# Optimization experiments

Measured on AMD Instinct MI355X. Metric: run time of the kernel, lower is better.

Reference implementation:

```python
import jax, jax.numpy as jnp
import numpy as np
from jax import lax

B, C, H, W = 4, 64, 64, 64
CH = C // 2  # edge_detect hidden channels
BN_EPS = 1e-5


def conv1x1(x, w, b):
    # x: (B,C,H,W), w: (O,C), b: (O,)
    return jnp.einsum('bchw,oc->bohw', x, w) + b[None, :, None, None]


def setup_inputs() -> dict:
    key = jax.random.key(0)
    ks = jax.random.split(key, 12)
    s = 1.0 / np.sqrt(C)
    inp = {
        'x': jax.random.normal(ks[0], (B, C, H, W), jnp.float32),
        'Wq': jax.random.normal(ks[1], (C, C), jnp.float32) * s,
        'bq': jnp.zeros((C,), jnp.float32),
        'Wk': jax.random.normal(ks[2], (C, C), jnp.float32) * s,
        'bk': jnp.zeros((C,), jnp.float32),
        'Wv': jax.random.normal(ks[3], (C, C), jnp.float32) * s,
        'bv': jnp.zeros((C,), jnp.float32),
        'We1': jax.random.normal(ks[4], (CH, C, 3, 3), jnp.float32) * (1.0 / np.sqrt(C * 9)),
        'be1': jnp.zeros((CH,), jnp.float32),
        'bn_w': jnp.ones((CH,), jnp.float32),
        'bn_b': jnp.zeros((CH,), jnp.float32),
        'bn_mean': jnp.zeros((CH,), jnp.float32),
        'bn_var': jnp.ones((CH,), jnp.float32),
        'We2': jax.random.normal(ks[5], (1, CH), jnp.float32) * (1.0 / np.sqrt(CH)),
        'be2': jnp.zeros((1,), jnp.float32),
        'gamma': jax.random.normal(ks[6], (1,), jnp.float32) * 0.1,
        'beta': jax.random.normal(ks[7], (1,), jnp.float32) * 0.1,
    }
    return inp


def reference(x, Wq, bq, Wk, bk, Wv, bv, We1, be1, bn_w, bn_b, bn_mean, bn_var, We2, be2, gamma, beta):
    b, c, h, w = x.shape
    hw = h * w
    q = conv1x1(x, Wq, bq).reshape(b, c, hw).transpose(0, 2, 1)  # (B,HW,C)
    k = conv1x1(x, Wk, bk).reshape(b, c, hw)                      # (B,C,HW)
    v = conv1x1(x, Wv, bv).reshape(b, c, hw)                      # (B,C,HW)

    energy = jnp.einsum('bnc,bcm->bnm', q, k)                      # (B,HW,HW)
    attention = jax.nn.softmax(energy, axis=-1)

    # edge_detect: 3x3 conv -> BN (eval stats) -> ReLU -> 1x1 conv -> sigmoid
    e = lax.conv_general_dilated(x, We1, (1, 1), 'SAME',
                                 dimension_numbers=('NCHW', 'OIHW', 'NCHW'))
    e = e + be1[None, :, None, None]
    e = (e - bn_mean[None, :, None, None]) * jax.lax.rsqrt(bn_var + BN_EPS)[None, :, None, None]
    e = e * bn_w[None, :, None, None] + bn_b[None, :, None, None]
    e = jax.nn.relu(e)
    e = conv1x1(e, We2, be2)                                       # (B,1,H,W)
    edge = jax.nn.sigmoid(e).reshape(b, 1, hw)                     # (B,1,HW)

    fa = attention * (1.0 + beta[0] * edge)                        # broadcast over query dim
    denom = jnp.maximum(jnp.sum(jnp.abs(fa), axis=2, keepdims=True), 1e-12)
    fa = fa / denom                                                # L1 renorm along keys

    out = jnp.einsum('bcm,bnm->bcn', v, fa).reshape(b, c, h, w)
    return gamma[0] * out + x
```

## Files before the change

### kernel.cpp

```cpp
#include <hip/hip_runtime.h>
#include <hip/hip_bf16.h>

typedef unsigned short u16;
typedef __attribute__((ext_vector_type(8))) __bf16 bf16x8;
typedef __attribute__((ext_vector_type(4))) float f32x4;
typedef __attribute__((ext_vector_type(16))) float f32x16;


#define NSPLIT 8

__device__ __forceinline__ u16 f2bf(float f) {
    unsigned u = __builtin_bit_cast(unsigned, f);
    u += 0x7FFFu + ((u >> 16) & 1u);
    return (u16)(u >> 16);
}
__device__ __forceinline__ float bf2f(u16 v) {
    unsigned u = ((unsigned)v) << 16;
    return __builtin_bit_cast(float, u);
}

__global__ __launch_bounds__(256) void qkv_edge_kernel(
    const float* __restrict__ x,
    const float* __restrict__ Wq, const float* __restrict__ bq,
    const float* __restrict__ Wk, const float* __restrict__ bk,
    const float* __restrict__ Wv, const float* __restrict__ bv,
    const float* __restrict__ We1, const float* __restrict__ be1,
    const float* __restrict__ bn_w, const float* __restrict__ bn_b,
    const float* __restrict__ bn_mean, const float* __restrict__ bn_var,
    const float* __restrict__ We2, const float* __restrict__ be2,
    const float* __restrict__ beta,
    u16* __restrict__ Qt, u16* __restrict__ Kt, u16* __restrict__ Vm,
    float* __restrict__ wkey)
{
    __shared__ __align__(16) u16 sm[33280];
    const int t = threadIdx.x;
    const int wv = t >> 6, lane = t & 63;
    const int quad = lane >> 4, l15 = lane & 15;

    if (blockIdx.x < 256) {
        u16* Wl   = sm;
        u16* xt_s = sm + 13824;
        u16* vt   = sm + 13824 + 4224;
        const int b = blockIdx.x >> 6;
        const int n0 = (blockIdx.x & 63) << 6;

        const float* Wmat[3] = {Wq, Wk, Wv};
#pragma unroll
        for (int m = 0; m < 3; ++m)
#pragma unroll
            for (int i = 0; i < 4; ++i) {
                int u = t + i * 256;
                float4 w4 = *reinterpret_cast<const float4*>(Wmat[m] + u * 4);
                int row = u >> 4, col = (u & 15) * 4;
                uint2 pk;
                pk.x = (unsigned)f2bf(w4.x) | ((unsigned)f2bf(w4.y) << 16);
                pk.y = (unsigned)f2bf(w4.z) | ((unsigned)f2bf(w4.w) << 16);
                *reinterpret_cast<uint2*>(&Wl[(m * 64 + row) * 72 + col]) = pk;
            }
        for (int i = 0; i < 16; ++i) {
            int lin = t + i * 256;
            int c = lin >> 6, nn = lin & 63;
            xt_s[nn * 66 + c] = f2bf(x[(size_t)(b * 64 + c) * 4096 + n0 + nn]);
        }
        __syncthreads();

        bf16x8 bx[2];
#pragma unroll
        for (int h = 0; h < 2; ++h)
            bx[h] = *reinterpret_cast<const bf16x8*>(
                &xt_s[(wv * 16 + l15) * 66 + h * 32 + quad * 8]);

        f32x4 d[3][4];
#pragma unroll
        for (int m = 0; m < 3; ++m)
#pragma unroll
            for (int mt = 0; mt < 4; ++mt) d[m][mt] = (f32x4){0.f, 0.f, 0.f, 0.f};

#pragma unroll
        for (int h = 0; h < 2; ++h)
#pragma unroll
            for (int m = 0; m < 3; ++m)
#pragma unroll
                for (int mt = 0; mt < 4; ++mt) {
                    bf16x8 af = *reinterpret_cast<const bf16x8*>(
                        &Wl[(m * 64 + mt * 16 + l15) * 72 + h * 32 + quad * 8]);
                    d[m][mt] = __builtin_amdgcn_mfma_f32_16x16x32_bf16(af, bx[h], d[m][mt], 0, 0, 0);
                }

        const float* bias[3] = {bq, bk, bv};
        const float L2E = 1.44269504f;
#pragma unroll
        for (int m = 0; m < 3; ++m)
#pragma unroll
            for (int mt = 0; mt < 4; ++mt) {
                float4 bi = *reinterpret_cast<const float4*>(bias[m] + mt * 16 + quad * 4);
                d[m][mt][0] += bi.x; d[m][mt][1] += bi.y; d[m][mt][2] += bi.z; d[m][mt][3] += bi.w;
                if (m == 0) {
                    d[m][mt][0] *= L2E; d[m][mt][1] *= L2E;
                    d[m][mt][2] *= L2E; d[m][mt][3] *= L2E;
                }
            }

        const int rowchunk = (n0 >> 4) + wv;
#pragma unroll
        for (int m = 0; m < 2; ++m) {
            u16* base = (m == 0 ? Qt : Kt) + (size_t)b * 262144;
#pragma unroll
            for (int mt = 0; mt < 4; ++mt) {
                uint2 pk;
                pk.x = (unsigned)f2bf(d[m][mt][0]) | ((unsigned)f2bf(d[m][mt][1]) << 16);
                pk.y = (unsigned)f2bf(d[m][mt][2]) | ((unsigned)f2bf(d[m][mt][3]) << 16);
                *reinterpret_cast<uint2*>(
                    base + ((size_t)(rowchunk * 8 + mt * 2 + (quad >> 1))) * 128 +
                    l15 * 8 + (quad & 1) * 4) = pk;
            }
        }
#pragma unroll
        for (int mt = 0; mt < 4; ++mt)
#pragma unroll
            for (int r = 0; r < 4; ++r)
                vt[(mt * 16 + quad * 4 + r) * 72 + wv * 16 + l15] = f2bf(d[2][mt][r]);
        __syncthreads();
        {
            u16* Vb_st = Vm + (size_t)b * 262144;
            const int kt = n0 >> 6;
#pragma unroll
            for (int i = 0; i < 2; ++i) {
                int unit = t + i * 256;
                int f = unit >> 7, hq = (unit >> 4) & 7, cl = unit & 15;
                const u16* src = &vt[(f * 16 + cl) * 72 + hq * 8];
                uint4 v4 = *reinterpret_cast<const uint4*>(src);
                *reinterpret_cast<uint4*>(
                    Vb_st + ((size_t)((kt * 4 + f) * 8 + hq)) * 128 + cl * 8) = v4;
            }
        }
    } else {
        u16* Ae_s = sm;
        u16* xr_s = sm + 18688;
        const int eb = blockIdx.x - 256;
        const int b = eb >> 6, h = eb & 63;

        if (t < 192) {
            int kh = t / 64, rem = t & 63;
            int col = (rem >> 5) * 65, ci2 = (rem & 31) * 2;
            *reinterpret_cast<unsigned*>(&xr_s[(kh * 66 + col) * 72 + ci2]) = 0u;
        }
#pragma unroll
        for (int i = 0; i < 18; ++i) {
            int u = t + i * 256;
            int ch = u / 144;
            int rem = u - ch * 144;
            int p = rem >> 4, cig = (rem & 15) * 4;
            const float* src = We1 + ch * 576 + cig * 9 + p;
            float a = src[0], b2 = src[9], c2 = src[18], d2 = src[27];
            uint2 pk;
            pk.x = (unsigned)f2bf(a) | ((unsigned)f2bf(b2) << 16);
            pk.y = (unsigned)f2bf(c2) | ((unsigned)f2bf(d2) << 16);
            *reinterpret_cast<uint2*>(&Ae_s[ch * 584 + p * 64 + cig]) = pk;
        }
#pragma unroll
        for (int i = 0; i < 12; ++i) {
            int u = t + i * 256;
            int w = u & 63, cig = (u >> 6) & 15, kh = u >> 10;
            int hs = h + kh - 1;
            float v0 = 0.f, v1 = 0.f, v2 = 0.f, v3 = 0.f;
            if ((unsigned)hs < 64u) {
                const float* src = x + ((size_t)(b * 64 + cig * 4) * 64 + hs) * 64 + w;
                v0 = src[0]; v1 = src[4096]; v2 = src[8192]; v3 = src[12288];
            }
            uint2 pk;
            pk.x = (unsigned)f2bf(v0) | ((unsigned)f2bf(v1) << 16);
            pk.y = (unsigned)f2bf(v2) | ((unsigned)f2bf(v3) << 16);
            *reinterpret_cast<uint2*>(&xr_s[(kh * 66 + w + 1) * 72 + cig * 4]) = pk;
        }
        __syncthreads();

        f32x4 e[2];
        e[0] = (f32x4){0.f, 0.f, 0.f, 0.f};
        e[1] = (f32x4){0.f, 0.f, 0.f, 0.f};
#pragma unroll
        for (int p = 0; p < 9; ++p) {
            const int kh = p / 3, kw = p - kh * 3;
#pragma unroll
            for (int half = 0; half < 2; ++half) {
                bf16x8 bfr = *reinterpret_cast<const bf16x8*>(
                    &xr_s[(kh * 66 + wv * 16 + l15 + kw) * 72 + half * 32 + quad * 8]);
#pragma unroll
                for (int mt = 0; mt < 2; ++mt) {
                    bf16x8 af = *reinterpret_cast<const bf16x8*>(
                        &Ae_s[(mt * 16 + l15) * 584 + p * 64 + half * 32 + quad * 8]);
                    e[mt] = __builtin_amdgcn_mfma_f32_16x16x32_bf16(af, bfr, e[mt], 0, 0, 0);
                }
            }
        }
        float partial = 0.f;
#pragma unroll
        for (int mt = 0; mt < 2; ++mt) {
            float4 bw = *reinterpret_cast<const float4*>(bn_w    + mt * 16 + quad * 4);
            float4 bb = *reinterpret_cast<const float4*>(bn_b    + mt * 16 + quad * 4);
            float4 bm = *reinterpret_cast<const float4*>(bn_mean + mt * 16 + quad * 4);
            float4 bv2 = *reinterpret_cast<const float4*>(bn_var + mt * 16 + quad * 4);
            float4 b1 = *reinterpret_cast<const float4*>(be1     + mt * 16 + quad * 4);
            float4 w2 = *reinterpret_cast<const float4*>(We2     + mt * 16 + quad * 4);
            float sc, sh;
            sc = bw.x * rsqrtf(bv2.x + 1e-5f); sh = (b1.x - bm.x) * sc + bb.x;
            partial += fmaxf(e[mt][0] * sc + sh, 0.f) * w2.x;
            sc = bw.y * rsqrtf(bv2.y + 1e-5f); sh = (b1.y - bm.y) * sc + bb.y;
            partial += fmaxf(e[mt][1] * sc + sh, 0.f) * w2.y;
            sc = bw.z * rsqrtf(bv2.z + 1e-5f); sh = (b1.z - bm.z) * sc + bb.z;
            partial += fmaxf(e[mt][2] * sc + sh, 0.f) * w2.z;
            sc = bw.w * rsqrtf(bv2.w + 1e-5f); sh = (b1.w - bm.w) * sc + bb.w;
            partial += fmaxf(e[mt][3] * sc + sh, 0.f) * w2.w;
        }
        partial += __shfl_xor(partial, 16);
        partial += __shfl_xor(partial, 32);
        if (lane < 16) {
            float s = partial + be2[0];
            float sg = 1.f / (1.f + __expf(-s));
            wkey[(size_t)b * 4096 + h * 64 + wv * 16 + lane] =
                __log2f(fmaxf(1.f + beta[0] * sg, 1e-20f)) - 17.3123405f;
        }
    }
}

__global__ __launch_bounds__(256, 2) void attn_kernel(
    const u16* __restrict__ Qt, const u16* __restrict__ Kt,
    const u16* __restrict__ Vm, const float* __restrict__ lwkey,
    u16* __restrict__ O_part, float* __restrict__ l_part)
{
    constexpr int KT_ITERS = 64 / NSPLIT;
    const int bid = ((blockIdx.x & 7) << 7) + (blockIdx.x >> 3);
    const int t = threadIdx.x;
    const int qi = bid / NSPLIT;
    const int split = bid % NSPLIT;
    const int b = qi >> 5;
    const int n0 = (qi & 31) << 7;
    const int wv = t >> 6, lane = t & 63;
    const int l31 = lane & 31, hi = lane >> 5;
    const int i4 = (lane >> 4) & 1, l15 = lane & 15;

    const int kvoff = i4 * 1024 + hi * 128 + l15 * 8;
    const u16* Qb = Qt + (size_t)b * 262144;
    const u16* Kp = Kt + (size_t)b * 262144 + (size_t)(split * KT_ITERS) * 4096 + kvoff;
    const u16* Vp = Vm + (size_t)b * 262144 + (size_t)(split * KT_ITERS) * 4096 + kvoff;
    const float* lwp = lwkey + (size_t)b * 4096 + (split * KT_ITERS) * 64 + hi * 4;

    bf16x8 qf[4];
#pragma unroll
    for (int kc = 0; kc < 4; ++kc)
        qf[kc] = __builtin_bit_cast(bf16x8, *reinterpret_cast<const uint4*>(
            Qb + (size_t)(((n0 >> 4) + wv * 2) * 1024) + kvoff + kc * 256));

    f32x16 o[2];
#pragma unroll
    for (int ct = 0; ct < 2; ++ct)
#pragma unroll
        for (int i = 0; i < 16; ++i) o[ct][i] = 0.f;
    float lacc = 0.f;

    for (int kt = 0; kt < KT_ITERS; ++kt) {
        uint4 pbu[2][2];
#pragma unroll
        for (int tl = 0; tl < 2; ++tl) {
            uint4 k0 = *reinterpret_cast<const uint4*>(Kp + tl * 2048);
            uint4 k1 = *reinterpret_cast<const uint4*>(Kp + tl * 2048 + 256);
            uint4 k2 = *reinterpret_cast<const uint4*>(Kp + tl * 2048 + 512);
            uint4 k3 = *reinterpret_cast<const uint4*>(Kp + tl * 2048 + 768);
            float4 lw0 = *reinterpret_cast<const float4*>(lwp + tl * 32);
            float4 lw1 = *reinterpret_cast<const float4*>(lwp + tl * 32 + 8);
            float4 lw2 = *reinterpret_cast<const float4*>(lwp + tl * 32 + 16);
            float4 lw3 = *reinterpret_cast<const float4*>(lwp + tl * 32 + 24);

            f32x16 s;
#pragma unroll
            for (int i = 0; i < 16; ++i) s[i] = 0.f;
            __builtin_amdgcn_s_setprio(1);
            s = __builtin_amdgcn_mfma_f32_32x32x16_bf16(__builtin_bit_cast(bf16x8, k0), qf[0], s, 0, 0, 0);
            s = __builtin_amdgcn_mfma_f32_32x32x16_bf16(__builtin_bit_cast(bf16x8, k1), qf[1], s, 0, 0, 0);
            s = __builtin_amdgcn_mfma_f32_32x32x16_bf16(__builtin_bit_cast(bf16x8, k2), qf[2], s, 0, 0, 0);
            s = __builtin_amdgcn_mfma_f32_32x32x16_bf16(__builtin_bit_cast(bf16x8, k3), qf[3], s, 0, 0, 0);
            __builtin_amdgcn_s_setprio(0);

            float p[16];
            p[0]  = exp2f(s[0]  + lw0.x); p[1]  = exp2f(s[1]  + lw0.y);
            p[2]  = exp2f(s[2]  + lw0.z); p[3]  = exp2f(s[3]  + lw0.w);
            p[4]  = exp2f(s[4]  + lw1.x); p[5]  = exp2f(s[5]  + lw1.y);
            p[6]  = exp2f(s[6]  + lw1.z); p[7]  = exp2f(s[7]  + lw1.w);
            p[8]  = exp2f(s[8]  + lw2.x); p[9]  = exp2f(s[9]  + lw2.y);
            p[10] = exp2f(s[10] + lw2.z); p[11] = exp2f(s[11] + lw2.w);
            p[12] = exp2f(s[12] + lw3.x); p[13] = exp2f(s[13] + lw3.y);
            p[14] = exp2f(s[14] + lw3.z); p[15] = exp2f(s[15] + lw3.w);
            float t0 = (p[0] + p[1]) + (p[2] + p[3]);
            float t1 = (p[4] + p[5]) + (p[6] + p[7]);
            float t2 = (p[8] + p[9]) + (p[10] + p[11]);
            float t3 = (p[12] + p[13]) + (p[14] + p[15]);
            lacc += (t0 + t1) + (t2 + t3);

#pragma unroll
            for (int kc2 = 0; kc2 < 2; ++kc2) {
                int a0, a1, b0, b1;
                asm("v_cvt_pk_bf16_f32 %0, %1, %2" : "=v"(a0) : "v"(p[kc2 * 8 + 0]), "v"(p[kc2 * 8 + 1]));
                asm("v_cvt_pk_bf16_f32 %0, %1, %2" : "=v"(a1) : "v"(p[kc2 * 8 + 2]), "v"(p[kc2 * 8 + 3]));
                asm("v_cvt_pk_bf16_f32 %0, %1, %2" : "=v"(b0) : "v"(p[kc2 * 8 + 4]), "v"(p[kc2 * 8 + 5]));
                asm("v_cvt_pk_bf16_f32 %0, %1, %2" : "=v"(b1) : "v"(p[kc2 * 8 + 6]), "v"(p[kc2 * 8 + 7]));
                auto swA = __builtin_amdgcn_permlane32_swap(a0, b0, false, false);
                auto swB = __builtin_amdgcn_permlane32_swap(a1, b1, false, false);
                uint4 fr;
                fr.x = (unsigned)swA[0];
                fr.y = (unsigned)swB[0];
                fr.z = (unsigned)swA[1];
                fr.w = (unsigned)swB[1];
                pbu[tl][kc2] = fr;
            }
        }

#pragma unroll
        for (int ct = 0; ct < 2; ++ct) {
            uint4 v0 = *reinterpret_cast<const uint4*>(Vp + ct * 2048);
            uint4 v1 = *reinterpret_cast<const uint4*>(Vp + ct * 2048 + 256);
            uint4 v2 = *reinterpret_cast<const uint4*>(Vp + ct * 2048 + 512);
            uint4 v3 = *reinterpret_cast<const uint4*>(Vp + ct * 2048 + 768);
            __builtin_amdgcn_s_setprio(1);
            o[ct] = __builtin_amdgcn_mfma_f32_32x32x16_bf16(__builtin_bit_cast(bf16x8, v0),
                        __builtin_bit_cast(bf16x8, pbu[0][0]), o[ct], 0, 0, 0);
            o[ct] = __builtin_amdgcn_mfma_f32_32x32x16_bf16(__builtin_bit_cast(bf16x8, v1),
                        __builtin_bit_cast(bf16x8, pbu[0][1]), o[ct], 0, 0, 0);
            o[ct] = __builtin_amdgcn_mfma_f32_32x32x16_bf16(__builtin_bit_cast(bf16x8, v2),
                        __builtin_bit_cast(bf16x8, pbu[1][0]), o[ct], 0, 0, 0);
            o[ct] = __builtin_amdgcn_mfma_f32_32x32x16_bf16(__builtin_bit_cast(bf16x8, v3),
                        __builtin_bit_cast(bf16x8, pbu[1][1]), o[ct], 0, 0, 0);
            __builtin_amdgcn_s_setprio(0);
        }
        Kp += 4096; Vp += 4096; lwp += 64;
    }

    float ltot = lacc + __shfl_xor(lacc, 32);
    if (lane < 32)
        l_part[(size_t)bid * 128 + wv * 32 + lane] = ltot;

    const size_t pbase = (size_t)bid * 8192;
    const int q = wv * 32 + l31;
#pragma unroll
    for (int ct = 0; ct < 2; ++ct)
#pragma unroll
        for (int g = 0; g < 4; ++g) {
            int w0, w1;
            asm("v_cvt_pk_bf16_f32 %0, %1, %2" : "=v"(w0) : "v"(o[ct][4 * g + 0]), "v"(o[ct][4 * g + 1]));
            asm("v_cvt_pk_bf16_f32 %0, %1, %2" : "=v"(w1) : "v"(o[ct][4 * g + 2]), "v"(o[ct][4 * g + 3]));
            uint2 pk2;
            pk2.x = (unsigned)w0;
            pk2.y = (unsigned)w1;
            *reinterpret_cast<uint2*>(
                &O_part[pbase + (size_t)(ct * 8 + g * 2 + hi) * 512 + q * 4]) = pk2;
        }
}

__global__ __launch_bounds__(256) void combine_kernel(
    const u16* __restrict__ O_part, const float* __restrict__ l_part,
    const float* __restrict__ x, const float* __restrict__ g_gamma,
    float* __restrict__ out)
{
    __shared__ float ot[32 * 65];
    __shared__ float ls[32];
    const int t = threadIdx.x;
    const int ab = blockIdx.x >> 2;
    const int sub = blockIdx.x & 3;
    const int b = ab >> 5;
    const int n0 = (ab & 31) << 7;
    const float gamma = g_gamma[0];

#pragma unroll
    for (int i = 0; i < 2; ++i) {
        int idx = t + i * 256;
        int c4 = idx >> 5, ql = idx & 31;
        float a0 = 0.f, a1 = 0.f, a2 = 0.f, a3 = 0.f;
#pragma unroll
        for (int s4 = 0; s4 < NSPLIT; ++s4) {
            uint2 u = *reinterpret_cast<const uint2*>(
                O_part + ((size_t)(ab * NSPLIT + s4)) * 8192 +
                (size_t)c4 * 512 + (sub * 32 + ql) * 4);
            a0 += bf2f((u16)(u.x & 0xFFFF));
            a1 += bf2f((u16)(u.x >> 16));
            a2 += bf2f((u16)(u.y & 0xFFFF));
            a3 += bf2f((u16)(u.y >> 16));
        }
        ot[ql * 65 + c4 * 4 + 0] = a0;
        ot[ql * 65 + c4 * 4 + 1] = a1;
        ot[ql * 65 + c4 * 4 + 2] = a2;
        ot[ql * 65 + c4 * 4 + 3] = a3;
    }
    if (t < 32) {
        float lsum = 0.f;
#pragma unroll
        for (int s4 = 0; s4 < NSPLIT; ++s4)
            lsum += l_part[((size_t)(ab * NSPLIT + s4)) * 128 + sub * 32 + t];
        ls[t] = gamma / fmaxf(lsum, 1e-30f);
    }
    __syncthreads();
    {
        const int c = t >> 2, seg = t & 3;
        const size_t gbase = ((size_t)(b * 64 + c)) * 4096 + n0 + sub * 32 + seg * 8;
#pragma unroll
        for (int j = 0; j < 2; ++j) {
            float4 xv = *reinterpret_cast<const float4*>(&x[gbase + j * 4]);
            float4 rv;
            int nl = seg * 8 + j * 4;
            rv.x = ot[(nl + 0) * 65 + c] * ls[nl + 0] + xv.x;
            rv.y = ot[(nl + 1) * 65 + c] * ls[nl + 1] + xv.y;
            rv.z = ot[(nl + 2) * 65 + c] * ls[nl + 2] + xv.z;
            rv.w = ot[(nl + 3) * 65 + c] * ls[nl + 3] + xv.w;
            *reinterpret_cast<float4*>(&out[gbase + j * 4]) = rv;
        }
    }
}

extern "C" void kernel_launch(void* const* d_in, const int* in_sizes, int n_in,
                              void* d_out, int out_size, void* d_ws, size_t ws_size,
                              hipStream_t stream) {
    const float* x      = (const float*)d_in[0];
    const float* Wq     = (const float*)d_in[1];
    const float* bq     = (const float*)d_in[2];
    const float* Wk     = (const float*)d_in[3];
    const float* bk     = (const float*)d_in[4];
    const float* Wv     = (const float*)d_in[5];
    const float* bv     = (const float*)d_in[6];
    const float* We1    = (const float*)d_in[7];
    const float* be1    = (const float*)d_in[8];
    const float* bn_w   = (const float*)d_in[9];
    const float* bn_b   = (const float*)d_in[10];
    const float* bn_mean= (const float*)d_in[11];
    const float* bn_var = (const float*)d_in[12];
    const float* We2    = (const float*)d_in[13];
    const float* be2    = (const float*)d_in[14];
    const float* gamma  = (const float*)d_in[15];
    const float* beta   = (const float*)d_in[16];

    char* ws = (char*)d_ws;
    const size_t KB = 1024, MB = 1024 * 1024;
    u16*   Qt     = (u16*)ws;
    u16*   Kt     = (u16*)(ws + 2 * MB);
    u16*   Vm     = (u16*)(ws + 4 * MB);
    float* lw     = (float*)(ws + 6 * MB);
    float* l_part = (float*)(ws + 6 * MB + 64 * KB);
    u16*   O_part = (u16*)(ws + 6 * MB + 576 * KB);

    float* out = (float*)d_out;

    qkv_edge_kernel<<<dim3(512), dim3(256), 0, stream>>>(
        x, Wq, bq, Wk, bk, Wv, bv, We1, be1, bn_w, bn_b, bn_mean, bn_var,
        We2, be2, beta, Qt, Kt, Vm, lw);
    attn_kernel<<<dim3(128 * NSPLIT), dim3(256), 0, stream>>>(
        Qt, Kt, Vm, lw, O_part, l_part);
    combine_kernel<<<dim3(512), dim3(256), 0, stream>>>(
        O_part, l_part, x, gamma, out);
}
```

Baseline: 136.9 us.

## Fold key log-weight into QK MFMA and prefetch K/V registers

The per-key log edge weight and the constant offset are now stored as an extra bf16 column block appended to K (5120-element tiles). A constant Q fragment multiplies it inside one additional MFMA, which removes the separate float loads and adds in the softmax loop. K and V fragments are also double-buffered in registers: the next tile's loads are issued right after the current MFMAs. The costs are one extra MFMA per tile, more registers, bf16 rounding of the log weight, and a redundant wraparound prefetch on the last iteration.

```diff
diff --git a/kernel.cpp b/kernel.cpp
--- a/kernel.cpp
+++ b/kernel.cpp
@@ -29,8 +29,7 @@
     const float* __restrict__ bn_mean, const float* __restrict__ bn_var,
     const float* __restrict__ We2, const float* __restrict__ be2,
     const float* __restrict__ beta,
-    u16* __restrict__ Qt, u16* __restrict__ Kt, u16* __restrict__ Vm,
-    float* __restrict__ wkey)
+    u16* __restrict__ Qt, u16* __restrict__ Kt, u16* __restrict__ Vm)
 {
     __shared__ __align__(16) u16 sm[33280];
     const int t = threadIdx.x;
@@ -102,16 +101,27 @@
             }
 
         const int rowchunk = (n0 >> 4) + wv;
-#pragma unroll
-        for (int m = 0; m < 2; ++m) {
-            u16* base = (m == 0 ? Qt : Kt) + (size_t)b * 262144;
+        {
+            u16* baseQ = Qt + (size_t)b * 262144;
 #pragma unroll
             for (int mt = 0; mt < 4; ++mt) {
                 uint2 pk;
-                pk.x = (unsigned)f2bf(d[m][mt][0]) | ((unsigned)f2bf(d[m][mt][1]) << 16);
-                pk.y = (unsigned)f2bf(d[m][mt][2]) | ((unsigned)f2bf(d[m][mt][3]) << 16);
+                pk.x = (unsigned)f2bf(d[0][mt][0]) | ((unsigned)f2bf(d[0][mt][1]) << 16);
+                pk.y = (unsigned)f2bf(d[0][mt][2]) | ((unsigned)f2bf(d[0][mt][3]) << 16);
                 *reinterpret_cast<uint2*>(
-                    base + ((size_t)(rowchunk * 8 + mt * 2 + (quad >> 1))) * 128 +
+                    baseQ + ((size_t)(rowchunk * 8 + mt * 2 + (quad >> 1))) * 128 +
+                    l15 * 8 + (quad & 1) * 4) = pk;
+            }
+        }
+        {
+            u16* baseK = Kt + (size_t)b * 327680 + (size_t)(n0 >> 6) * 5120;
+#pragma unroll
+            for (int mt = 0; mt < 4; ++mt) {
+                uint2 pk;
+                pk.x = (unsigned)f2bf(d[1][mt][0]) | ((unsigned)f2bf(d[1][mt][1]) << 16);
+                pk.y = (unsigned)f2bf(d[1][mt][2]) | ((unsigned)f2bf(d[1][mt][3]) << 16);
+                *reinterpret_cast<uint2*>(
+                    baseK + (size_t)(wv * 8 + mt * 2 + (quad >> 1)) * 128 +
                     l15 * 8 + (quad & 1) * 4) = pk;
             }
         }
@@ -217,15 +227,22 @@
         if (lane < 16) {
             float s = partial + be2[0];
             float sg = 1.f / (1.f + __expf(-s));
-            wkey[(size_t)b * 4096 + h * 64 + wv * 16 + lane] =
-                __log2f(fmaxf(1.f + beta[0] * sg, 1e-20f)) - 17.3123405f;
+            float lwp = __log2f(fmaxf(1.f + beta[0] * sg, 1e-20f));
+            u16* k5 = Kt + (size_t)b * 327680 + (size_t)h * 5120 + 4096 +
+                      (wv >> 1) * 512 + (wv & 1) * 256 + lane * 8;
+            uint4 st0;
+            st0.x = (unsigned)f2bf(lwp) | 0x3F800000u;
+            st0.y = 0u; st0.z = 0u; st0.w = 0u;
+            *reinterpret_cast<uint4*>(k5) = st0;
+            uint4 z; z.x = 0u; z.y = 0u; z.z = 0u; z.w = 0u;
+            *reinterpret_cast<uint4*>(k5 + 128) = z;
         }
     }
 }
 
 __global__ __launch_bounds__(256, 2) void attn_kernel(
     const u16* __restrict__ Qt, const u16* __restrict__ Kt,
-    const u16* __restrict__ Vm, const float* __restrict__ lwkey,
+    const u16* __restrict__ Vm,
     u16* __restrict__ O_part, float* __restrict__ l_part)
 {
     constexpr int KT_ITERS = 64 / NSPLIT;
@@ -240,16 +257,35 @@
     const int i4 = (lane >> 4) & 1, l15 = lane & 15;
 
     const int kvoff = i4 * 1024 + hi * 128 + l15 * 8;
-    const u16* Qb = Qt + (size_t)b * 262144;
-    const u16* Kp = Kt + (size_t)b * 262144 + (size_t)(split * KT_ITERS) * 4096 + kvoff;
-    const u16* Vp = Vm + (size_t)b * 262144 + (size_t)(split * KT_ITERS) * 4096 + kvoff;
-    const float* lwp = lwkey + (size_t)b * 4096 + (split * KT_ITERS) * 64 + hi * 4;
+    const int k5off = i4 * 256 + hi * 128 + l15 * 8;
+    const u16* Qb  = Qt + (size_t)b * 262144;
+    const u16* Ksp = Kt + (size_t)b * 327680 + (size_t)(split * KT_ITERS) * 5120;
+    const u16* Vsp = Vm + (size_t)b * 262144 + (size_t)(split * KT_ITERS) * 4096;
 
     bf16x8 qf[4];
 #pragma unroll
     for (int kc = 0; kc < 4; ++kc)
         qf[kc] = __builtin_bit_cast(bf16x8, *reinterpret_cast<const uint4*>(
             Qb + (size_t)(((n0 >> 4) + wv * 2) * 1024) + kvoff + kc * 256));
+    uint4 qc5u;
+    qc5u.x = hi ? 0u : 0xC18A3F80u;
+    qc5u.y = 0u; qc5u.z = 0u; qc5u.w = 0u;
+    const bf16x8 qc5 = __builtin_bit_cast(bf16x8, qc5u);
+
+    uint4 kf[2][5];
+    uint4 vf[2][4];
+#pragma unroll
+    for (int tl = 0; tl < 2; ++tl) {
+#pragma unroll
+        for (int kc = 0; kc < 4; ++kc)
+            kf[tl][kc] = *reinterpret_cast<const uint4*>(Ksp + tl * 2048 + kc * 256 + kvoff);
+        kf[tl][4] = *reinterpret_cast<const uint4*>(Ksp + 4096 + tl * 512 + k5off);
+    }
+#pragma unroll
+    for (int ct = 0; ct < 2; ++ct)
+#pragma unroll
+        for (int kc = 0; kc < 4; ++kc)
+            vf[ct][kc] = *reinterpret_cast<const uint4*>(Vsp + ct * 2048 + kc * 256 + kvoff);
 
     f32x16 o[2];
 #pragma unroll
@@ -259,43 +295,46 @@
     float lacc = 0.f;
 
     for (int kt = 0; kt < KT_ITERS; ++kt) {
+        f32x16 s0, s1;
+#pragma unroll
+        for (int i = 0; i < 16; ++i) { s0[i] = 0.f; s1[i] = 0.f; }
+        __builtin_amdgcn_s_setprio(1);
+        s0 = __builtin_amdgcn_mfma_f32_32x32x16_bf16(__builtin_bit_cast(bf16x8, kf[0][4]), qc5,   s0, 0, 0, 0);
+        s0 = __builtin_amdgcn_mfma_f32_32x32x16_bf16(__builtin_bit_cast(bf16x8, kf[0][0]), qf[0], s0, 0, 0, 0);
+        s0 = __builtin_amdgcn_mfma_f32_32x32x16_bf16(__builtin_bit_cast(bf16x8, kf[0][1]), qf[1], s0, 0, 0, 0);
+        s0 = __builtin_amdgcn_mfma_f32_32x32x16_bf16(__builtin_bit_cast(bf16x8, kf[0][2]), qf[2], s0, 0, 0, 0);
+        s0 = __builtin_amdgcn_mfma_f32_32x32x16_bf16(__builtin_bit_cast(bf16x8, kf[0][3]), qf[3], s0, 0, 0, 0);
+        s1 = __builtin_amdgcn_mfma_f32_32x32x16_bf16(__builtin_bit_cast(bf16x8, kf[1][4]), qc5,   s1, 0, 0, 0);
+        s1 = __builtin_amdgcn_mfma_f32_32x32x16_bf16(__builtin_bit_cast(bf16x8, kf[1][0]), qf[0], s1, 0, 0, 0);
+        s1 = __builtin_amdgcn_mfma_f32_32x32x16_bf16(__builtin_bit_cast(bf16x8, kf[1][1]), qf[1], s1, 0, 0, 0);
+        s1 = __builtin_amdgcn_mfma_f32_32x32x16_bf16(__builtin_bit_cast(bf16x8, kf[1][2]), qf[2], s1, 0, 0, 0);
+        s1 = __builtin_amdgcn_mfma_f32_32x32x16_bf16(__builtin_bit_cast(bf16x8, kf[1][3]), qf[3], s1, 0, 0, 0);
+        __builtin_amdgcn_s_setprio(0);
+
+        const int ktn = (kt + 1) & (KT_ITERS - 1);
+        {
+            const u16* Kn = Ksp + (size_t)ktn * 5120;
+#pragma unroll
+            for (int tl = 0; tl < 2; ++tl) {
+#pragma unroll
+                for (int kc = 0; kc < 4; ++kc)
+                    kf[tl][kc] = *reinterpret_cast<const uint4*>(Kn + tl * 2048 + kc * 256 + kvoff);
+                kf[tl][4] = *reinterpret_cast<const uint4*>(Kn + 4096 + tl * 512 + k5off);
+            }
+        }
+
         uint4 pbu[2][2];
 #pragma unroll
         for (int tl = 0; tl < 2; ++tl) {
-            uint4 k0 = *reinterpret_cast<const uint4*>(Kp + tl * 2048);
-            uint4 k1 = *reinterpret_cast<const uint4*>(Kp + tl * 2048 + 256);
-            uint4 k2 = *reinterpret_cast<const uint4*>(Kp + tl * 2048 + 512);
-            uint4 k3 = *reinterpret_cast<const uint4*>(Kp + tl * 2048 + 768);
-            float4 lw0 = *reinterpret_cast<const float4*>(lwp + tl * 32);
-            float4 lw1 = *reinterpret_cast<const float4*>(lwp + tl * 32 + 8);
-            float4 lw2 = *reinterpret_cast<const float4*>(lwp + tl * 32 + 16);
-            float4 lw3 = *reinterpret_cast<const float4*>(lwp + tl * 32 + 24);
-
-            f32x16 s;
-#pragma unroll
-            for (int i = 0; i < 16; ++i) s[i] = 0.f;
-            __builtin_amdgcn_s_setprio(1);
-            s = __builtin_amdgcn_mfma_f32_32x32x16_bf16(__builtin_bit_cast(bf16x8, k0), qf[0], s, 0, 0, 0);
-            s = __builtin_amdgcn_mfma_f32_32x32x16_bf16(__builtin_bit_cast(bf16x8, k1), qf[1], s, 0, 0, 0);
-            s = __builtin_amdgcn_mfma_f32_32x32x16_bf16(__builtin_bit_cast(bf16x8, k2), qf[2], s, 0, 0, 0);
-            s = __builtin_amdgcn_mfma_f32_32x32x16_bf16(__builtin_bit_cast(bf16x8, k3), qf[3], s, 0, 0, 0);
-            __builtin_amdgcn_s_setprio(0);
-
+            const f32x16& sv = tl ? s1 : s0;
             float p[16];
-            p[0]  = exp2f(s[0]  + lw0.x); p[1]  = exp2f(s[1]  + lw0.y);
-            p[2]  = exp2f(s[2]  + lw0.z); p[3]  = exp2f(s[3]  + lw0.w);
-            p[4]  = exp2f(s[4]  + lw1.x); p[5]  = exp2f(s[5]  + lw1.y);
-            p[6]  = exp2f(s[6]  + lw1.z); p[7]  = exp2f(s[7]  + lw1.w);
-            p[8]  = exp2f(s[8]  + lw2.x); p[9]  = exp2f(s[9]  + lw2.y);
-            p[10] = exp2f(s[10] + lw2.z); p[11] = exp2f(s[11] + lw2.w);
-            p[12] = exp2f(s[12] + lw3.x); p[13] = exp2f(s[13] + lw3.y);
-            p[14] = exp2f(s[14] + lw3.z); p[15] = exp2f(s[15] + lw3.w);
+#pragma unroll
+            for (int i = 0; i < 16; ++i) p[i] = exp2f(sv[i]);
             float t0 = (p[0] + p[1]) + (p[2] + p[3]);
             float t1 = (p[4] + p[5]) + (p[6] + p[7]);
             float t2 = (p[8] + p[9]) + (p[10] + p[11]);
             float t3 = (p[12] + p[13]) + (p[14] + p[15]);
             lacc += (t0 + t1) + (t2 + t3);
-
 #pragma unroll
             for (int kc2 = 0; kc2 < 2; ++kc2) {
                 int a0, a1, b0, b1;
@@ -314,24 +353,28 @@
             }
         }
 
+        __builtin_amdgcn_s_setprio(1);
 #pragma unroll
         for (int ct = 0; ct < 2; ++ct) {
-            uint4 v0 = *reinterpret_cast<const uint4*>(Vp + ct * 2048);
-            uint4 v1 = *reinterpret_cast<const uint4*>(Vp + ct * 2048 + 256);
-            uint4 v2 = *reinterpret_cast<const uint4*>(Vp + ct * 2048 + 512);
-            uint4 v3 = *reinterpret_cast<const uint4*>(Vp + ct * 2048 + 768);
-            __builtin_amdgcn_s_setprio(1);
-            o[ct] = __builtin_amdgcn_mfma_f32_32x32x16_bf16(__builtin_bit_cast(bf16x8, v0),
+            o[ct] = __builtin_amdgcn_mfma_f32_32x32x16_bf16(__builtin_bit_cast(bf16x8, vf[ct][0]),
                         __builtin_bit_cast(bf16x8, pbu[0][0]), o[ct], 0, 0, 0);
-            o[ct] = __builtin_amdgcn_mfma_f32_32x32x16_bf16(__builtin_bit_cast(bf16x8, v1),
+            o[ct] = __builtin_amdgcn_mfma_f32_32x32x16_bf16(__builtin_bit_cast(bf16x8, vf[ct][1]),
                         __builtin_bit_cast(bf16x8, pbu[0][1]), o[ct], 0, 0, 0);
-            o[ct] = __builtin_amdgcn_mfma_f32_32x32x16_bf16(__builtin_bit_cast(bf16x8, v2),
+            o[ct] = __builtin_amdgcn_mfma_f32_32x32x16_bf16(__builtin_bit_cast(bf16x8, vf[ct][2]),
                         __builtin_bit_cast(bf16x8, pbu[1][0]), o[ct], 0, 0, 0);
-            o[ct] = __builtin_amdgcn_mfma_f32_32x32x16_bf16(__builtin_bit_cast(bf16x8, v3),
+            o[ct] = __builtin_amdgcn_mfma_f32_32x32x16_bf16(__builtin_bit_cast(bf16x8, vf[ct][3]),
                         __builtin_bit_cast(bf16x8, pbu[1][1]), o[ct], 0, 0, 0);
-            __builtin_amdgcn_s_setprio(0);
-        }
-        Kp += 4096; Vp += 4096; lwp += 64;
+        }
+        __builtin_amdgcn_s_setprio(0);
+
+        {
+            const u16* Vn = Vsp + (size_t)ktn * 4096;
+#pragma unroll
+            for (int ct = 0; ct < 2; ++ct)
+#pragma unroll
+                for (int kc = 0; kc < 4; ++kc)
+                    vf[ct][kc] = *reinterpret_cast<const uint4*>(Vn + ct * 2048 + kc * 256 + kvoff);
+        }
     }
 
     float ltot = lacc + __shfl_xor(lacc, 32);
@@ -436,21 +479,20 @@
     const float* beta   = (const float*)d_in[16];
 
     char* ws = (char*)d_ws;
-    const size_t KB = 1024, MB = 1024 * 1024;
+    const size_t MB = 1024 * 1024;
     u16*   Qt     = (u16*)ws;
     u16*   Kt     = (u16*)(ws + 2 * MB);
-    u16*   Vm     = (u16*)(ws + 4 * MB);
-    float* lw     = (float*)(ws + 6 * MB);
-    float* l_part = (float*)(ws + 6 * MB + 64 * KB);
-    u16*   O_part = (u16*)(ws + 6 * MB + 576 * KB);
+    u16*   Vm     = (u16*)(ws + 5 * MB);
+    float* l_part = (float*)(ws + 7 * MB);
+    u16*   O_part = (u16*)(ws + 8 * MB);
 
     float* out = (float*)d_out;
 
     qkv_edge_kernel<<<dim3(512), dim3(256), 0, stream>>>(
         x, Wq, bq, Wk, bk, Wv, bv, We1, be1, bn_w, bn_b, bn_mean, bn_var,
-        We2, be2, beta, Qt, Kt, Vm, lw);
+        We2, be2, beta, Qt, Kt, Vm);
     attn_kernel<<<dim3(128 * NSPLIT), dim3(256), 0, stream>>>(
-        Qt, Kt, Vm, lw, O_part, l_part);
+        Qt, Kt, Vm, O_part, l_part);
     combine_kernel<<<dim3(512), dim3(256), 0, stream>>>(
         O_part, l_part, x, gamma, out);
 }
```

Result: no change. 136.0 us (-0.6%).
